# Kernel optimization log

Hardware: AMD Instinct MI355X
Metric: run time of the kernel (lower is better)

## Reference

```python
import jax, jax.numpy as jnp
import numpy as np

B, T, C = 2, 2048, 2048
H, Hk, D = 32, 4, 64
N_REP = H // Hk
THETA = 10000.0


def _rope_tables():
    inv_freq = 1.0 / (THETA ** (np.arange(0, D, 2, dtype=np.float64) / D))  # [D/2]
    t = np.arange(T, dtype=np.float64)
    freqs = np.outer(t, inv_freq)                # [T, D/2]
    emb = np.repeat(freqs, 2, axis=-1)           # interleaved [T, D]
    return jnp.asarray(np.cos(emb), jnp.float32), jnp.asarray(np.sin(emb), jnp.float32)


def setup_inputs() -> dict:
    key = jax.random.key(0)
    kx, kq, kk, kv, ko = jax.random.split(key, 5)
    scale = 0.02
    x = jax.random.normal(kx, (B, T, C), jnp.float32)
    wq = jax.random.normal(kq, (H * D, C), jnp.float32) * scale
    wk = jax.random.normal(kk, (Hk * D, C), jnp.float32) * scale
    wv = jax.random.normal(kv, (Hk * D, C), jnp.float32) * scale
    wo = jax.random.normal(ko, (C, H * D), jnp.float32) * scale
    cos, sin = _rope_tables()
    return {"x": x, "cos": cos, "sin": sin, "wq": wq, "wk": wk, "wv": wv, "wo": wo}


def _apply_rope(x, cos, sin):
    # x: [B, h, T, D]; cos/sin: [T, D] interleaved
    x1 = x[..., 0::2]
    x2 = x[..., 1::2]
    rot = jnp.stack([-x2, x1], axis=-1).reshape(x.shape)
    return x * cos[None, None] + rot * sin[None, None]


def reference(x, cos, sin, wq, wk, wv, wo):
    q = (x @ wq.T).reshape(B, T, H, D).transpose(0, 2, 1, 3)    # [B,H,T,D]
    k = (x @ wk.T).reshape(B, T, Hk, D).transpose(0, 2, 1, 3)   # [B,Hk,T,D]
    v = (x @ wv.T).reshape(B, T, Hk, D).transpose(0, 2, 1, 3)   # [B,Hk,T,D]
    q = _apply_rope(q, cos, sin)
    k = _apply_rope(k, cos, sin)
    # new_cache = (k, v) pre-repeat
    kr = jnp.repeat(k, N_REP, axis=1)                            # [B,H,T,D]
    vr = jnp.repeat(v, N_REP, axis=1)
    scores = jnp.einsum('bhtd,bhsd->bhts', q, kr) / jnp.sqrt(jnp.float32(D))
    mask = jnp.tril(jnp.ones((T, T), dtype=bool))                # causal (kv_cache is None)
    scores = jnp.where(mask, scores, jnp.finfo(scores.dtype).min)
    attn = jax.nn.softmax(scores, axis=-1)
    o = jnp.einsum('bhts,bhsd->bhtd', attn, vr)
    o = o.transpose(0, 2, 1, 3).reshape(B, T, H * D)
    return (o @ wo.T, k, v)
```

## Files before the change

kernel.cpp:

```cpp
#include <hip/hip_runtime.h>
#include <hip/hip_bf16.h>

#define B_ 2
#define T_ 2048
#define C_ 2048
#define H_ 32
#define HK_ 4
#define D_ 64

typedef __attribute__((ext_vector_type(4)))  float f32x4;
typedef __attribute__((ext_vector_type(2)))  float f32x2;
typedef __attribute__((ext_vector_type(16))) float f32x16;
typedef __attribute__((ext_vector_type(8)))  short bf16x8;

static __device__ __forceinline__ unsigned short f2bf(float f) {
  union { __hip_bfloat16 h; unsigned short s; } u;
  u.h = __float2bfloat16(f);
  return u.s;
}
static __device__ __forceinline__ float bf2f(unsigned short s) {
  union { unsigned int u; float f; } u; u.u = ((unsigned int)s) << 16; return u.f;
}
static __device__ __forceinline__ unsigned int cvtpk(float lo, float hi) {
  unsigned int r;
  asm("v_cvt_pk_bf16_f32 %0, %1, %2" : "=v"(r) : "v"(lo), "v"(hi));
  return r;
}

#define GLD16(gp, lp) __builtin_amdgcn_global_load_lds( \
    (const __attribute__((address_space(1))) unsigned int*)(gp), \
    (__attribute__((address_space(3))) unsigned int*)(unsigned int)(uintptr_t)(lp), 16, 0, 0)

__global__ void conv_all(const float* __restrict__ x,  const float* __restrict__ wq,
                         const float* __restrict__ wk, const float* __restrict__ wv,
                         const float* __restrict__ wo,
                         unsigned short* __restrict__ x_bf,
                         unsigned short* __restrict__ wqkv,
                         unsigned short* __restrict__ wo_bf) {
  const int i = blockIdx.x * blockDim.x + threadIdx.x;
  const float* src;
  unsigned short* dst;
  int off;
  if (i < 2097152)      { src = x;  dst = x_bf;                  off = i; }
  else if (i < 3145728) { src = wq; dst = wqkv;                  off = i - 2097152; }
  else if (i < 3276800) { src = wk; dst = wqkv + 2048 * 2048;    off = i - 3145728; }
  else if (i < 3407872) { src = wv; dst = wqkv + 2304 * 2048;    off = i - 3276800; }
  else                  { src = wo; dst = wo_bf;                 off = i - 3407872; }
  f32x4 v = *(const f32x4*)(src + 4 * (size_t)off);
  ushort4 o;
  o.x = f2bf(v[0]); o.y = f2bf(v[1]); o.z = f2bf(v[2]); o.w = f2bf(v[3]);
  *(ushort4*)(dst + 4 * (size_t)off) = o;
}

__global__ __launch_bounds__(256, 3)
void gemm_qkv(const unsigned short* __restrict__ A, const unsigned short* __restrict__ W,
              int M, int N, int K,
              const float* __restrict__ cosT, const float* __restrict__ sinT,
              unsigned short* __restrict__ qb, unsigned short* __restrict__ kbf,
              unsigned short* __restrict__ vtb, float* __restrict__ koutf,
              float* __restrict__ voutf) {
  __shared__ unsigned short As[3][128 * 32];
  __shared__ unsigned short Ws[3][128 * 32];

  const int tid  = threadIdx.x;
  const int lane = tid & 63;
  const int w    = tid >> 6;
  const int wm   = w >> 1, wn = w & 1;
  const int g    = lane >> 4;
  const int lr   = lane & 15;

  const int gx   = gridDim.x;
  const int flat = blockIdx.y * gx + blockIdx.x;
  const int cpx  = (gx * gridDim.y) >> 3;
  const int swzb = (flat & 7) * cpx + (flat >> 3);
  const int bm   = (swzb / gx) * 128;
  const int bn   = (swzb % gx) * 128;

  const int srow = tid >> 2;
  const int sc   = (tid & 3) ^ (srow & 3);
  const unsigned short* Ag = A + (size_t)(bm + srow) * K + sc * 8;
  const unsigned short* Wg = W + (size_t)(bn + srow) * K + sc * 8;

#define STAGEQ(buf, k0) do { \
    GLD16(Ag + (k0),                  &As[buf][       w * 512]); \
    GLD16(Ag + (size_t)64 * K + (k0), &As[buf][2048 + w * 512]); \
    GLD16(Wg + (k0),                  &Ws[buf][       w * 512]); \
    GLD16(Wg + (size_t)64 * K + (k0), &Ws[buf][2048 + w * 512]); \
  } while (0)

  f32x4 acc[4][4] = {};

  const int nt = K >> 5;
  STAGEQ(0, 0);
  STAGEQ(1, 32);

  for (int t = 0; t < nt; ++t) {
    if (t + 1 < nt) asm volatile("s_waitcnt vmcnt(4)" ::: "memory");
    else            asm volatile("s_waitcnt vmcnt(0)" ::: "memory");
    asm volatile("s_barrier" ::: "memory");

    if (t + 2 < nt) {
      const int nb = (t + 2) % 3;
      STAGEQ(nb, (size_t)(t + 2) * 32);
    }

    const unsigned short* At = &As[t % 3][0];
    const unsigned short* Wt = &Ws[t % 3][0];

    bf16x8 af[4], wf[4];
#pragma unroll
    for (int m = 0; m < 4; m++) {
      const int row = wm * 64 + m * 16 + lr;
      af[m] = *(const bf16x8*)&At[row * 32 + ((g ^ (row & 3)) << 3)];
    }
#pragma unroll
    for (int n = 0; n < 4; n++) {
      const int row = wn * 64 + n * 16 + lr;
      wf[n] = *(const bf16x8*)&Wt[row * 32 + ((g ^ (row & 3)) << 3)];
    }
    __builtin_amdgcn_s_setprio(1);
#pragma unroll
    for (int m = 0; m < 4; m++)
#pragma unroll
      for (int n = 0; n < 4; n++)
        acc[m][n] = __builtin_amdgcn_mfma_f32_16x16x32_bf16(af[m], wf[n], acc[m][n], 0, 0, 0);
    __builtin_amdgcn_s_setprio(0);
  }
#undef STAGEQ

  const int seg = (bn < 2048) ? 0 : (bn < 2304 ? 1 : 2);
#pragma unroll
  for (int m = 0; m < 4; m++) {
#pragma unroll
    for (int n = 0; n < 4; n++) {
      const int col = bn + wn * 64 + n * 16 + lr;
      const int d   = col & 63;
#pragma unroll
      for (int r = 0; r < 4; r++) {
        const int row = bm + wm * 64 + m * 16 + g * 4 + r;
        const int tt  = row & (T_ - 1);
        const int bb  = row >> 11;
        const float val = acc[m][n][r];
        if (seg == 2) {
          const int hk = (col >> 6) - 36;
          const size_t idx = ((size_t)(bb * HK_ + hk) * T_ + tt) * D_ + d;
          voutf[idx] = val;
          const int tm   = tt & 15;
          const int tpos = (tt & ~15) | ((tm & 3) + ((tm >> 3) << 2) + ((tm & 4) << 1));
          vtb[((size_t)(bb * HK_ + hk) * D_ + d) * T_ + tpos] = f2bf(val);
        } else {
          const float cs = cosT[tt * D_ + d];
          const float sn = sinT[tt * D_ + d];
          const float other = __shfl_xor(val, 1);
          const float o = val * cs + ((lr & 1) ? other : -other) * sn;
          if (seg == 0) {
            const int h = col >> 6;
            qb[((size_t)(bb * H_ + h) * T_ + tt) * D_ + d] = f2bf(o);
          } else {
            const int hk = (col >> 6) - 32;
            const size_t idx = ((size_t)(bb * HK_ + hk) * T_ + tt) * D_ + d;
            koutf[idx] = o;
            kbf[idx]   = f2bf(o);
          }
        }
      }
    }
  }
}

__global__ __launch_bounds__(256, 3)
void gemm_wo(const unsigned short* __restrict__ A, const unsigned short* __restrict__ W,
             float* __restrict__ Cf, int M, int N, int K) {
  __shared__ unsigned short As[3][128 * 32];
  __shared__ unsigned short Ws[3][128 * 32];

  const int tid  = threadIdx.x;
  const int lane = tid & 63;
  const int w    = tid >> 6;
  const int wm   = w >> 1, wn = w & 1;
  const int g    = lane >> 4;
  const int lr   = lane & 15;

  const int bm = blockIdx.y * 128;
  const int bn = blockIdx.x * 128;

  const int srow = tid >> 2;
  const int sc   = (tid & 3) ^ (srow & 3);
  const unsigned short* Ag = A + (size_t)(bm + srow) * K + sc * 8;
  const unsigned short* Wg = W + (size_t)(bn + srow) * K + sc * 8;

#define STAGEW(buf, k0) do { \
    GLD16(Ag + (k0),                  &As[buf][       w * 512]); \
    GLD16(Ag + (size_t)64 * K + (k0), &As[buf][2048 + w * 512]); \
    GLD16(Wg + (k0),                  &Ws[buf][       w * 512]); \
    GLD16(Wg + (size_t)64 * K + (k0), &Ws[buf][2048 + w * 512]); \
  } while (0)

  f32x4 acc[4][4] = {};

  const int nt = K >> 5;
  STAGEW(0, 0);
  STAGEW(1, 32);

  for (int t = 0; t < nt; ++t) {
    if (t + 1 < nt) asm volatile("s_waitcnt vmcnt(4)" ::: "memory");
    else            asm volatile("s_waitcnt vmcnt(0)" ::: "memory");
    asm volatile("s_barrier" ::: "memory");

    if (t + 2 < nt) {
      const int nb = (t + 2) % 3;
      STAGEW(nb, (size_t)(t + 2) * 32);
    }

    const unsigned short* At = &As[t % 3][0];
    const unsigned short* Wt = &Ws[t % 3][0];

    bf16x8 af[4], wf[4];
#pragma unroll
    for (int m = 0; m < 4; m++) {
      const int row = wm * 64 + m * 16 + lr;
      af[m] = *(const bf16x8*)&At[row * 32 + ((g ^ (row & 3)) << 3)];
    }
#pragma unroll
    for (int n = 0; n < 4; n++) {
      const int row = wn * 64 + n * 16 + lr;
      wf[n] = *(const bf16x8*)&Wt[row * 32 + ((g ^ (row & 3)) << 3)];
    }
    __builtin_amdgcn_s_setprio(1);
#pragma unroll
    for (int m = 0; m < 4; m++)
#pragma unroll
      for (int n = 0; n < 4; n++)
        acc[m][n] = __builtin_amdgcn_mfma_f32_16x16x32_bf16(af[m], wf[n], acc[m][n], 0, 0, 0);
    __builtin_amdgcn_s_setprio(0);
  }
#undef STAGEW

#pragma unroll
  for (int m = 0; m < 4; m++) {
    const int row = bm + wm * 64 + m * 16 + g * 4;
#pragma unroll
    for (int n = 0; n < 4; n++) {
      const int col = bn + wn * 64 + n * 16 + lr;
#pragma unroll
      for (int r = 0; r < 4; r++)
        Cf[(size_t)(row + r) * N + col] = acc[m][n][r];
    }
  }
}

static __device__ __forceinline__ void attn_qstep(
    const unsigned short* __restrict__ Kt, const unsigned short* __restrict__ Vt,
    const bf16x8 (&qf)[4], f32x16& o0, f32x16& o1,
    float& m, float& l, float& c1,
    const int qrow, const int kb0, const bool last,
    const int qi, const int hi, const int swz) {
  const float SC   = 0.125f * 1.44269504089f;
  const float THRR = 44.3614195f;
  const int  qtop  = (qrow & ~31) + 31;
  const bool has1  = (kb0 + 32 <= qtop);

  f32x16 st0 = {}, st1 = {};
  __builtin_amdgcn_s_setprio(1);
#pragma unroll
  for (int c = 0; c < 4; c++) {
    bf16x8 kf = *(const bf16x8*)&Kt[qi * 64 + (((hi + 2 * c) ^ swz) << 3)];
    st0 = __builtin_amdgcn_mfma_f32_32x32x16_bf16(kf, qf[c], st0, 0, 0, 0);
  }
  if (!last || has1) {
#pragma unroll
    for (int c = 0; c < 4; c++) {
      bf16x8 kf = *(const bf16x8*)&Kt[(32 + qi) * 64 + (((hi + 2 * c) ^ swz) << 3)];
      st1 = __builtin_amdgcn_mfma_f32_32x32x16_bf16(kf, qf[c], st1, 0, 0, 0);
    }
  }
  __builtin_amdgcn_s_setprio(0);

  if (last) {
#pragma unroll
    for (int r = 0; r < 16; ++r) {
      const int key = kb0 + (r & 3) + 8 * (r >> 2) + 4 * hi;
      st0[r] = (key      <= qrow) ? st0[r] : -1e30f;
      st1[r] = (key + 32 <= qrow) ? st1[r] : -1e30f;
    }
  }

  float tmax = fmaxf(st0[0], st0[1]);
#pragma unroll
  for (int r = 2; r < 16; ++r) tmax = fmaxf(tmax, st0[r]);
#pragma unroll
  for (int r = 0; r < 16; ++r) tmax = fmaxf(tmax, st1[r]);
  tmax = fmaxf(tmax, __shfl_xor(tmax, 32));

  if (!__all(tmax <= m + THRR)) {
    const float mnew = fmaxf(m, tmax);
    const float al   = __builtin_amdgcn_exp2f((m - mnew) * SC);
#pragma unroll
    for (int r = 0; r < 16; ++r) { o0[r] *= al; o1[r] *= al; }
    l *= al;
    m  = mnew;
    c1 = -m * SC;
  }

  float sum = 0.f;
#pragma unroll
  for (int r = 0; r < 16; ++r) { float pv = __builtin_amdgcn_exp2f(__builtin_fmaf(st0[r], SC, c1)); st0[r] = pv; sum += pv; }
#pragma unroll
  for (int r = 0; r < 16; ++r) { float pv = __builtin_amdgcn_exp2f(__builtin_fmaf(st1[r], SC, c1)); st1[r] = pv; sum += pv; }
  sum += __shfl_xor(sum, 32);
  l += sum;

  union U8 { bf16x8 v; unsigned int u[4]; };
  U8 pf[4];
#pragma unroll
  for (int j = 0; j < 4; ++j) {
    pf[0].u[j] = cvtpk(st0[2 * j],     st0[2 * j + 1]);
    pf[1].u[j] = cvtpk(st0[8 + 2 * j], st0[8 + 2 * j + 1]);
    pf[2].u[j] = cvtpk(st1[2 * j],     st1[2 * j + 1]);
    pf[3].u[j] = cvtpk(st1[8 + 2 * j], st1[8 + 2 * j + 1]);
  }

  const int ncf = (!last || has1) ? 4 : 2;
  __builtin_amdgcn_s_setprio(1);
#pragma unroll
  for (int dh = 0; dh < 2; ++dh) {
    const unsigned short* Vrow = &Vt[(dh * 32 + qi) * 64];
    f32x16 oc = dh ? o1 : o0;
#pragma unroll
    for (int c = 0; c < 4; ++c) {
      if (c >= ncf) break;
      bf16x8 vf = *(const bf16x8*)&Vrow[(((2 * c + hi) ^ swz) << 3)];
      oc = __builtin_amdgcn_mfma_f32_32x32x16_bf16(vf, pf[c].v, oc, 0, 0, 0);
    }
    if (dh) o1 = oc; else o0 = oc;
  }
  __builtin_amdgcn_s_setprio(0);
}

__global__ __launch_bounds__(512, 2)
void gqa_attn5(const unsigned short* __restrict__ qb,
               const unsigned short* __restrict__ kb,
               const unsigned short* __restrict__ vt,
               unsigned short* __restrict__ ob) {
  __shared__ unsigned short Ks[3][4096];
  __shared__ unsigned short Vs[3][4096];

  const int tid  = threadIdx.x;
  const int lane = tid & 63;
  const int w    = tid >> 6;
  const int qi   = lane & 31;
  const int hi   = lane >> 5;

  const int go = blockIdx.x & 7;
  const int pp = blockIdx.x >> 3;
  const int b  = go >> 2;
  const int hk = go & 3;
  const int h  = hk * 8 + w;
  const int bh = b * H_ + h;

  const int qbaseA = (63 - pp) * 32;
  const int qbaseB = pp * 32;
  const int qrowA  = qbaseA + qi;
  const int qrowB  = qbaseB + qi;

  bf16x8 qfA[4], qfB[4];
  {
    const unsigned short* qpA = qb + ((size_t)bh * T_ + qrowA) * D_ + 8 * hi;
    const unsigned short* qpB = qb + ((size_t)bh * T_ + qrowB) * D_ + 8 * hi;
#pragma unroll
    for (int c = 0; c < 4; c++) {
      qfA[c] = *(const bf16x8*)(qpA + 16 * c);
      qfB[c] = *(const bf16x8*)(qpB + 16 * c);
    }
  }

  const int srow   = lane >> 3;
  const int schunk = (lane & 7) ^ srow;
  const int krow   = 8 * w + srow;
  const unsigned short* gK = kb + (size_t)(b * HK_ + hk) * T_ * D_ + (size_t)krow * D_ + schunk * 8;
  const unsigned short* gV = vt + (size_t)(b * HK_ + hk) * D_ * T_ + (size_t)krow * T_ + schunk * 8;
  unsigned short* ldsK = &Ks[0][w * 512];
  unsigned short* ldsV = &Vs[0][w * 512];

#define STAGE_KV(pbuf, kk0) do { \
    GLD16(gK + (size_t)(kk0) * D_, ldsK + (pbuf) * 4096); \
    GLD16(gV + (kk0),              ldsV + (pbuf) * 4096); \
  } while (0)

  f32x16 o0A = {}, o1A = {}, o0B = {}, o1B = {};
  float mA = -1e30f, lA = 0.f, c1A = 0.f;
  float mB = -1e30f, lB = 0.f, c1B = 0.f;
  const int swz = qi & 7;

  const int ntA = ((qbaseA + 31) >> 6) + 1;
  const int ntB = ((qbaseB + 31) >> 6) + 1;

  STAGE_KV(0, 0);
  if (ntA > 1) STAGE_KV(1, 64);

  int p = 0;
  for (int it = 0; it < ntA; ++it) {
    const int kb0 = it * 64;

    asm volatile("s_waitcnt lgkmcnt(0)" ::: "memory");
    if (it + 1 < ntA) asm volatile("s_waitcnt vmcnt(2)" ::: "memory");
    else              asm volatile("s_waitcnt vmcnt(0)" ::: "memory");
    asm volatile("s_barrier" ::: "memory");
    if (it + 2 < ntA) STAGE_KV((p + 2 > 2) ? p - 1 : p + 2, kb0 + 128);

    const unsigned short* Kt = &Ks[0][0] + p * 4096;
    const unsigned short* Vt = &Vs[0][0] + p * 4096;

    attn_qstep(Kt, Vt, qfA, o0A, o1A, mA, lA, c1A, qrowA, kb0, it == ntA - 1, qi, hi, swz);
    if (it < ntB)
      attn_qstep(Kt, Vt, qfB, o0B, o1B, mB, lB, c1B, qrowB, kb0, it == ntB - 1, qi, hi, swz);

    p = (p > 1) ? 0 : p + 1;
  }

  const float invA = 1.0f / lA;
  const float invB = 1.0f / lB;
  unsigned short* orowA = ob + (size_t)(b * T_ + qrowA) * (H_ * D_) + h * D_;
  unsigned short* orowB = ob + (size_t)(b * T_ + qrowB) * (H_ * D_) + h * D_;
#pragma unroll
  for (int dh = 0; dh < 2; ++dh) {
    const f32x16 ovA = dh ? o1A : o0A;
    const f32x16 ovB = dh ? o1B : o0B;
#pragma unroll
    for (int rg = 0; rg < 4; ++rg) {
      const int d0 = 32 * dh + 8 * rg + 4 * hi;
      ushort4 pkA, pkB;
      pkA.x = f2bf(ovA[4 * rg + 0] * invA);
      pkA.y = f2bf(ovA[4 * rg + 1] * invA);
      pkA.z = f2bf(ovA[4 * rg + 2] * invA);
      pkA.w = f2bf(ovA[4 * rg + 3] * invA);
      pkB.x = f2bf(ovB[4 * rg + 0] * invB);
      pkB.y = f2bf(ovB[4 * rg + 1] * invB);
      pkB.z = f2bf(ovB[4 * rg + 2] * invB);
      pkB.w = f2bf(ovB[4 * rg + 3] * invB);
      *(ushort4*)(orowA + d0) = pkA;
      *(ushort4*)(orowB + d0) = pkB;
    }
  }
#undef STAGE_KV
}

extern "C" void kernel_launch(void* const* d_in, const int* in_sizes, int n_in,
                              void* d_out, int out_size, void* d_ws, size_t ws_size,
                              hipStream_t stream) {
  const float* x    = (const float*)d_in[0];
  const float* cosT = (const float*)d_in[1];
  const float* sinT = (const float*)d_in[2];
  const float* wq   = (const float*)d_in[3];
  const float* wk   = (const float*)d_in[4];
  const float* wv   = (const float*)d_in[5];
  const float* wo   = (const float*)d_in[6];

  float* y    = (float*)d_out;
  float* kout = (float*)d_out + (size_t)B_ * T_ * C_;
  float* vout = kout + (size_t)B_ * HK_ * T_ * D_;

  char* ws = (char*)d_ws;
  unsigned short* x_bf = (unsigned short*)(ws);
  unsigned short* o_bf = x_bf;
  unsigned short* wqkv = (unsigned short*)(ws + 16777216);
  unsigned short* q_bf = (unsigned short*)(ws + 27262976);
  unsigned short* k_bf = (unsigned short*)(ws + 44040192);
  unsigned short* v_t  = (unsigned short*)(ws + 46137344);
  unsigned short* wo_bf= (unsigned short*)(ws + 48234496);

  const int M = B_ * T_;

  conv_all<<<17408, 256, 0, stream>>>(x, wq, wk, wv, wo, x_bf, wqkv, wo_bf);

  gemm_qkv<<<dim3(2560 / 128, M / 128), 256, 0, stream>>>(
      x_bf, wqkv, M, 2560, C_, cosT, sinT, q_bf, k_bf, v_t, kout, vout);

  gqa_attn5<<<256, 512, 0, stream>>>(q_bf, k_bf, v_t, o_bf);

  gemm_wo<<<dim3(C_ / 128, M / 128), 256, 0, stream>>>(o_bf, wo_bf, y, M, C_, H_ * D_);
}
```

Measured before the change: 188.3 us.

## Defer Q RoPE into attention kernel and store raw Q row-major

The QKV GEMM epilogue no longer applies RoPE to Q and scatters it into head-major layout. It writes unrotated bf16 Q in the GEMM's natural row-major [B*T, 2560] layout, and the attention kernel applies RoPE to its Q fragments at load time using the cos/sin tables. The block-swizzle tile ordering in the QKV GEMM is also removed. The aim is to cut epilogue shuffles and table loads and to make Q stores contiguous. In exchange, Q is rounded to bf16 before rotation and then again after, which adds rounding error, and the attention prologue does extra work and strided loads.

```diff
diff --git a/kernel.cpp b/kernel.cpp
--- a/kernel.cpp
+++ b/kernel.cpp
@@ -56,7 +56,7 @@
 void gemm_qkv(const unsigned short* __restrict__ A, const unsigned short* __restrict__ W,
               int M, int N, int K,
               const float* __restrict__ cosT, const float* __restrict__ sinT,
-              unsigned short* __restrict__ qb, unsigned short* __restrict__ kbf,
+              unsigned short* __restrict__ qkvb, unsigned short* __restrict__ kbf,
               unsigned short* __restrict__ vtb, float* __restrict__ koutf,
               float* __restrict__ voutf) {
   __shared__ unsigned short As[3][128 * 32];
@@ -69,12 +69,8 @@
   const int g    = lane >> 4;
   const int lr   = lane & 15;
 
-  const int gx   = gridDim.x;
-  const int flat = blockIdx.y * gx + blockIdx.x;
-  const int cpx  = (gx * gridDim.y) >> 3;
-  const int swzb = (flat & 7) * cpx + (flat >> 3);
-  const int bm   = (swzb / gx) * 128;
-  const int bn   = (swzb % gx) * 128;
+  const int bm = blockIdx.y * 128;
+  const int bn = blockIdx.x * 128;
 
   const int srow = tid >> 2;
   const int sc   = (tid & 3) ^ (srow & 3);
@@ -129,34 +125,43 @@
 #undef STAGEQ
 
   const int seg = (bn < 2048) ? 0 : (bn < 2304 ? 1 : 2);
-#pragma unroll
-  for (int m = 0; m < 4; m++) {
-#pragma unroll
-    for (int n = 0; n < 4; n++) {
-      const int col = bn + wn * 64 + n * 16 + lr;
-      const int d   = col & 63;
-#pragma unroll
-      for (int r = 0; r < 4; r++) {
-        const int row = bm + wm * 64 + m * 16 + g * 4 + r;
-        const int tt  = row & (T_ - 1);
-        const int bb  = row >> 11;
-        const float val = acc[m][n][r];
-        if (seg == 2) {
-          const int hk = (col >> 6) - 36;
-          const size_t idx = ((size_t)(bb * HK_ + hk) * T_ + tt) * D_ + d;
-          voutf[idx] = val;
-          const int tm   = tt & 15;
-          const int tpos = (tt & ~15) | ((tm & 3) + ((tm >> 3) << 2) + ((tm & 4) << 1));
-          vtb[((size_t)(bb * HK_ + hk) * D_ + d) * T_ + tpos] = f2bf(val);
-        } else {
-          const float cs = cosT[tt * D_ + d];
-          const float sn = sinT[tt * D_ + d];
-          const float other = __shfl_xor(val, 1);
-          const float o = val * cs + ((lr & 1) ? other : -other) * sn;
-          if (seg == 0) {
-            const int h = col >> 6;
-            qb[((size_t)(bb * H_ + h) * T_ + tt) * D_ + d] = f2bf(o);
+  if (seg == 0) {
+#pragma unroll
+    for (int m = 0; m < 4; m++) {
+      const int row = bm + wm * 64 + m * 16 + g * 4;
+#pragma unroll
+      for (int n = 0; n < 4; n++) {
+        const int col = bn + wn * 64 + n * 16 + lr;
+#pragma unroll
+        for (int r = 0; r < 4; r++)
+          qkvb[(size_t)(row + r) * 2560 + col] = f2bf(acc[m][n][r]);
+      }
+    }
+  } else {
+#pragma unroll
+    for (int m = 0; m < 4; m++) {
+#pragma unroll
+      for (int n = 0; n < 4; n++) {
+        const int col = bn + wn * 64 + n * 16 + lr;
+        const int d   = col & 63;
+#pragma unroll
+        for (int r = 0; r < 4; r++) {
+          const int row = bm + wm * 64 + m * 16 + g * 4 + r;
+          const int tt  = row & (T_ - 1);
+          const int bb  = row >> 11;
+          const float val = acc[m][n][r];
+          if (seg == 2) {
+            const int hk = (col >> 6) - 36;
+            const size_t idx = ((size_t)(bb * HK_ + hk) * T_ + tt) * D_ + d;
+            voutf[idx] = val;
+            const int tm   = tt & 15;
+            const int tpos = (tt & ~15) | ((tm & 3) + ((tm >> 3) << 2) + ((tm & 4) << 1));
+            vtb[((size_t)(bb * HK_ + hk) * D_ + d) * T_ + tpos] = f2bf(val);
           } else {
+            const float cs = cosT[tt * D_ + d];
+            const float sn = sinT[tt * D_ + d];
+            const float other = __shfl_xor(val, 1);
+            const float o = val * cs + ((lr & 1) ? other : -other) * sn;
             const int hk = (col >> 6) - 32;
             const size_t idx = ((size_t)(bb * HK_ + hk) * T_ + tt) * D_ + d;
             koutf[idx] = o;
@@ -338,7 +343,8 @@
 }
 
 __global__ __launch_bounds__(512, 2)
-void gqa_attn5(const unsigned short* __restrict__ qb,
+void gqa_attn6(const unsigned short* __restrict__ qkv,
+               const float* __restrict__ cosT, const float* __restrict__ sinT,
                const unsigned short* __restrict__ kb,
                const unsigned short* __restrict__ vt,
                unsigned short* __restrict__ ob) {
@@ -365,12 +371,34 @@
 
   bf16x8 qfA[4], qfB[4];
   {
-    const unsigned short* qpA = qb + ((size_t)bh * T_ + qrowA) * D_ + 8 * hi;
-    const unsigned short* qpB = qb + ((size_t)bh * T_ + qrowB) * D_ + 8 * hi;
+    const unsigned short* qpA = qkv + ((size_t)(b * T_ + qrowA)) * 2560 + h * D_ + 8 * hi;
+    const unsigned short* qpB = qkv + ((size_t)(b * T_ + qrowB)) * 2560 + h * D_ + 8 * hi;
+    const float* cA = cosT + qrowA * D_ + 8 * hi;
+    const float* sA = sinT + qrowA * D_ + 8 * hi;
+    const float* cB = cosT + qrowB * D_ + 8 * hi;
+    const float* sB = sinT + qrowB * D_ + 8 * hi;
 #pragma unroll
     for (int c = 0; c < 4; c++) {
-      qfA[c] = *(const bf16x8*)(qpA + 16 * c);
-      qfB[c] = *(const bf16x8*)(qpB + 16 * c);
+      const bf16x8 ra = *(const bf16x8*)(qpA + 16 * c);
+      const bf16x8 rb = *(const bf16x8*)(qpB + 16 * c);
+#pragma unroll
+      for (int j = 0; j < 4; j++) {
+        const int dd = 16 * c + 2 * j;
+        {
+          const float x1 = bf2f((unsigned short)ra[2 * j]);
+          const float x2 = bf2f((unsigned short)ra[2 * j + 1]);
+          const float cc = cA[dd], ss = sA[dd];
+          qfA[c][2 * j]     = (short)f2bf(x1 * cc - x2 * ss);
+          qfA[c][2 * j + 1] = (short)f2bf(x2 * cc + x1 * ss);
+        }
+        {
+          const float x1 = bf2f((unsigned short)rb[2 * j]);
+          const float x2 = bf2f((unsigned short)rb[2 * j + 1]);
+          const float cc = cB[dd], ss = sB[dd];
+          qfB[c][2 * j]     = (short)f2bf(x1 * cc - x2 * ss);
+          qfB[c][2 * j + 1] = (short)f2bf(x2 * cc + x1 * ss);
+        }
+      }
     }
   }
 
@@ -461,22 +489,22 @@
   float* vout = kout + (size_t)B_ * HK_ * T_ * D_;
 
   char* ws = (char*)d_ws;
-  unsigned short* x_bf = (unsigned short*)(ws);
-  unsigned short* o_bf = x_bf;
-  unsigned short* wqkv = (unsigned short*)(ws + 16777216);
-  unsigned short* q_bf = (unsigned short*)(ws + 27262976);
-  unsigned short* k_bf = (unsigned short*)(ws + 44040192);
-  unsigned short* v_t  = (unsigned short*)(ws + 46137344);
-  unsigned short* wo_bf= (unsigned short*)(ws + 48234496);
+  unsigned short* x_bf   = (unsigned short*)(ws);
+  unsigned short* o_bf   = x_bf;
+  unsigned short* wqkv   = (unsigned short*)(ws + 16777216);
+  unsigned short* qkv_bf = (unsigned short*)(ws + 27262976);
+  unsigned short* k_bf   = (unsigned short*)(ws + 48234496);
+  unsigned short* v_t    = (unsigned short*)(ws + 50331648);
+  unsigned short* wo_bf  = (unsigned short*)(ws + 52428800);
 
   const int M = B_ * T_;
 
   conv_all<<<17408, 256, 0, stream>>>(x, wq, wk, wv, wo, x_bf, wqkv, wo_bf);
 
   gemm_qkv<<<dim3(2560 / 128, M / 128), 256, 0, stream>>>(
-      x_bf, wqkv, M, 2560, C_, cosT, sinT, q_bf, k_bf, v_t, kout, vout);
-
-  gqa_attn5<<<256, 512, 0, stream>>>(q_bf, k_bf, v_t, o_bf);
+      x_bf, wqkv, M, 2560, C_, cosT, sinT, qkv_bf, k_bf, v_t, kout, vout);
+
+  gqa_attn6<<<256, 512, 0, stream>>>(qkv_bf, cosT, sinT, k_bf, v_t, o_bf);
 
   gemm_wo<<<dim3(C_ / 128, M / 128), 256, 0, stream>>>(o_bf, wo_bf, y, M, C_, H_ * D_);
 }
```

After: 201.2 us. 1.07x slower.
